# Performance work log

Hardware: AMD Instinct MI355X
Metric: run time of the kernel (lower is better)

The kernel has to match this reference:

```python
import jax, jax.numpy as jnp
import numpy as np

TAU = 0.1
EPS_FREQ = 1e-06
EPS_DENOM = 1e-12


def _l2norm(x, eps=1e-12):
    # matches F.normalize(p=2, dim=-1)
    n = jnp.linalg.norm(x, axis=-1, keepdims=True)
    return x / jnp.maximum(n, eps)


def setup_inputs() -> dict:
    key = jax.random.key(0)
    k1, k2, k3, k4, k5 = jax.random.split(key, 5)
    N, D, C = 4096, 128, 64
    return {
        "protos": jax.random.normal(k1, (C, D), dtype=jnp.float32),
        "proj2": jax.random.normal(k2, (N, D), dtype=jnp.float32),
        "target2": jax.random.randint(k3, (N,), 0, C, dtype=jnp.int64),
        "proj3": jax.random.normal(k4, (N, D), dtype=jnp.float32),
        "target3": jax.random.randint(k5, (N,), 0, C, dtype=jnp.int64),
    }


def reference(protos, proj2, target2, proj3, target3):
    feats = _l2norm(jnp.concatenate([proj2, proj3], axis=0))        # [M, D]
    labels = jnp.concatenate([target2, target3], axis=0)             # [M]
    protos_n = _l2norm(protos)                                       # [C, D]
    M = feats.shape[0]
    C = protos_n.shape[0]

    sim = jnp.matmul(feats, feats.T) / TAU                           # [M, M]
    proto_sim = jnp.matmul(feats, protos_n.T) / TAU                  # [M, C]

    eye = jnp.eye(M, dtype=bool)
    exp_sim = jnp.where(eye, 0.0, jnp.exp(sim))                      # diag masked to -inf -> exp 0
    exp_proto = jnp.exp(proto_sim)

    match = labels[:, None] == labels[None, :]                       # [M, M]
    numer_region = jnp.sum(exp_sim * match, axis=1)                  # [M]
    numer_proto = jnp.take_along_axis(exp_proto, labels[:, None], axis=1)[:, 0]
    numer = numer_region + numer_proto

    # bincount(labels ++ arange(C)) == per-class count + 1
    cls_freq = jnp.zeros((C,), dtype=jnp.float32).at[labels].add(1.0) + 1.0 + EPS_FREQ
    feat_w = cls_freq[labels]                                        # [M], per-row weight

    denom_region = jnp.sum(exp_sim, axis=1) / feat_w                 # row-constant weight; diag already 0
    denom_proto = jnp.sum(exp_proto / cls_freq[None, :], axis=1)
    denom = denom_region + denom_proto

    loss = -jnp.log(numer / (denom + EPS_DENOM))
    return jnp.mean(loss)
```

## Files before the change

kernel.cpp:

```cpp
#include <hip/hip_runtime.h>
#include <math.h>
#include <stdint.h>

#define D    128
#define CCLS 64
#define CH   16

typedef _Float16 f16x8 __attribute__((ext_vector_type(8)));
typedef float    f32x4 __attribute__((ext_vector_type(4)));

__device__ __forceinline__ float wave_reduce_sum(float v) {
    #pragma unroll
    for (int off = 32; off > 0; off >>= 1) v += __shfl_xor(v, off, 64);
    return v;
}

__device__ __forceinline__ void gload_lds16(const void* g, void* l) {
    __builtin_amdgcn_global_load_lds(
        (const __attribute__((address_space(1))) uint32_t*)g,
        (__attribute__((address_space(3))) uint32_t*)l, 16, 0, 0);
}
__device__ __forceinline__ void gload_lds4(const void* g, void* l) {
    __builtin_amdgcn_global_load_lds(
        (const __attribute__((address_space(1))) uint32_t*)g,
        (__attribute__((address_space(3))) uint32_t*)l, 4, 0, 0);
}

__global__ void norm_kernel(const float* __restrict__ protos,
                            const float* __restrict__ proj2,
                            const float* __restrict__ proj3,
                            const int* __restrict__ t2, const int* __restrict__ t3,
                            _Float16* __restrict__ ftile, int* __restrict__ labs,
                            float* __restrict__ cls_freq, float* __restrict__ loss_sum,
                            int* __restrict__ ticket, int N, int M) {
    const float SCL = 3.8017368953f;
    int w = threadIdx.x >> 6;
    int lane = threadIdx.x & 63;
    int row = blockIdx.x * (blockDim.x >> 6) + w;
    const int MT = M + 128;

    if (blockIdx.x == 0) {
        __shared__ int h[CCLS];
        int t = threadIdx.x;
        if (t < CCLS) h[t] = 0;
        if (t == 0) { loss_sum[0] = 0.f; ticket[0] = 0; }
        __syncthreads();
        for (int i = t; i < M; i += blockDim.x) {
            int lab = (i < N) ? t2[i] : t3[i - N];
            atomicAdd(&h[lab], 1);
        }
        __syncthreads();
        if (t < CCLS) cls_freq[t] = (float)h[t] + 1.0f + 1e-6f;
    }

    if (row < MT) {
        const float* src = nullptr;
        if (row < M)             src = (row < N) ? proj2 + (size_t)row * D
                                                 : proj3 + (size_t)(row - N) * D;
        else if (row < M + CCLS) src = protos + (size_t)(row - M) * D;
        float2 v = {0.f, 0.f};
        if (src) v = ((const float2*)src)[lane];
        float ss = wave_reduce_sum(v.x * v.x + v.y * v.y);
        float scale = src ? SCL / fmaxf(sqrtf(ss), 1e-12f) : 0.f;
        _Float16 h0 = (_Float16)(v.x * scale), h1 = (_Float16)(v.y * scale);
        int k0 = 2 * lane;
        size_t off = ((size_t)(row >> 4) * 16 + (k0 >> 3)) * 128 + (row & 15) * 8 + (k0 & 7);
        ftile[off] = h0; ftile[off + 1] = h1;
        if (row < M && lane == 0)
            labs[row] = (row < N) ? t2[row] : t3[row - N];
    }
}

__global__ __launch_bounds__(256, 4)
void sim_kernel(const _Float16* __restrict__ ftile,
                const int* __restrict__ labs,
                const float* __restrict__ cls_freq,
                float* __restrict__ nPart, float* __restrict__ dPart,
                float* __restrict__ rp, int M) {
    __shared__ _Float16 sbuf[2][8320];

    const int panel = blockIdx.x;
    const int chunk = blockIdx.y;
    const int t = threadIdx.x;
    const int w = t >> 6, lane = t & 63;
    const int g = lane >> 4, li = lane & 15;
    const int lo = g * 128 + li * 8;
    const int rtA = panel * 8 + w * 2;
    const int nS = (M / 64) / CH;
    const int sBase = chunk * nS;
    const int row0 = panel * 128 + 32 * w + li;
    const int rl0 = labs[row0];
    const int rl1 = labs[row0 + 16];

    f16x8 a[2][4];
    #pragma unroll
    for (int m = 0; m < 2; ++m)
        #pragma unroll
        for (int kt = 0; kt < 4; ++kt)
            a[m][kt] = *(const f16x8*)(ftile + (size_t)(rtA + m) * 2048 + kt * 512 + lo);

    float rn[2] = {0.f, 0.f}, rd[2] = {0.f, 0.f};
    float rpacc[2] = {0.f, 0.f};

    #define STAGE(buf, s)                                                        \
        {                                                                        \
            const char* bsrc_ = (const char*)ftile + (size_t)(s) * 16384;        \
            char* dst_ = (char*)&sbuf[(buf)][0];                                 \
            _Pragma("unroll")                                                    \
            for (int q = 0; q < 4; ++q) {                                        \
                int j_ = w * 4 + q;                                              \
                gload_lds16(bsrc_ + (size_t)j_ * 1024 + lane * 16,               \
                            dst_ + (size_t)j_ * 1024);                           \
            }                                                                    \
            if (w == 0)                                                          \
                gload_lds4((const char*)labs + (size_t)(s) * 256 + lane * 4,     \
                           dst_ + 16384);                                        \
        }

    STAGE(0, sBase);
    __syncthreads();
    int cur = 0;

    const int diagS = 2 * panel + (w >> 1);
    const int nD0 = 2 * (w & 1);

    for (int si = 0; si < nS; ++si) {
        const int s = sBase + si;
        if (si + 1 < nS) STAGE(cur ^ 1, sBase + si + 1);

        const _Float16* Bl = &sbuf[cur][0];
        const int* clabL = (const int*)&sbuf[cur][8192];
        const bool isDiag = (s == diagS);

        #pragma unroll
        for (int n = 0; n < 4; ++n) {
            f16x8 bn[4];
            #pragma unroll
            for (int kt = 0; kt < 4; ++kt)
                bn[kt] = *(const f16x8*)(Bl + n * 2048 + kt * 512 + lo);

            f32x4 acc[2];
            #pragma unroll
            for (int m = 0; m < 2; ++m)
                #pragma unroll
                for (int r = 0; r < 4; ++r) acc[m][r] = 0.f;

            #pragma unroll
            for (int kt = 0; kt < 4; ++kt)
                #pragma unroll
                for (int m = 0; m < 2; ++m)
                    acc[m] = __builtin_amdgcn_mfma_f32_16x16x32_f16(bn[kt], a[m][kt], acc[m], 0, 0, 0);

            if (isDiag) {
                #pragma unroll
                for (int m = 0; m < 2; ++m)
                    #pragma unroll
                    for (int r = 0; r < 4; ++r)
                        acc[m][r] = (n == nD0 + m && 4 * g + r == li) ? -1e5f : acc[m][r];
            }

            int4 c4 = *(const int4*)(clabL + 16 * n + 4 * g);
            #pragma unroll
            for (int m = 0; m < 2; ++m) {
                float e0 = __builtin_amdgcn_exp2f(acc[m][0]);
                float e1 = __builtin_amdgcn_exp2f(acc[m][1]);
                float e2 = __builtin_amdgcn_exp2f(acc[m][2]);
                float e3 = __builtin_amdgcn_exp2f(acc[m][3]);
                const int rl = m ? rl1 : rl0;
                rd[m] += e0 + e1 + e2 + e3;
                rn[m] += (c4.x == rl) ? e0 : 0.f;
                rn[m] += (c4.y == rl) ? e1 : 0.f;
                rn[m] += (c4.z == rl) ? e2 : 0.f;
                rn[m] += (c4.w == rl) ? e3 : 0.f;
            }
        }

        __syncthreads();
        cur ^= 1;
    }

    if (chunk == 0) {
        const int rbp = M >> 4;
        #pragma unroll
        for (int n = 0; n < 4; ++n) {
            f16x8 bn[4];
            #pragma unroll
            for (int kt = 0; kt < 4; ++kt)
                bn[kt] = *(const f16x8*)(ftile + (size_t)(rbp + n) * 2048 + kt * 512 + lo);
            f32x4 acc[2];
            #pragma unroll
            for (int m = 0; m < 2; ++m)
                #pragma unroll
                for (int r = 0; r < 4; ++r) acc[m][r] = 0.f;
            #pragma unroll
            for (int kt = 0; kt < 4; ++kt)
                #pragma unroll
                for (int m = 0; m < 2; ++m)
                    acc[m] = __builtin_amdgcn_mfma_f32_16x16x32_f16(bn[kt], a[m][kt], acc[m], 0, 0, 0);

            f32x4 fr = *(const f32x4*)(cls_freq + 16 * n + 4 * g);
            const int c0 = 16 * n + 4 * g;
            #pragma unroll
            for (int m = 0; m < 2; ++m) {
                float e0 = __builtin_amdgcn_exp2f(acc[m][0]);
                float e1 = __builtin_amdgcn_exp2f(acc[m][1]);
                float e2 = __builtin_amdgcn_exp2f(acc[m][2]);
                float e3 = __builtin_amdgcn_exp2f(acc[m][3]);
                const int rl = m ? rl1 : rl0;
                rpacc[m] += e0 / fr[0] + e1 / fr[1] + e2 / fr[2] + e3 / fr[3];
                rn[m] += (c0 + 0 == rl) ? e0 : 0.f;
                rn[m] += (c0 + 1 == rl) ? e1 : 0.f;
                rn[m] += (c0 + 2 == rl) ? e2 : 0.f;
                rn[m] += (c0 + 3 == rl) ? e3 : 0.f;
            }
        }
    }

    #pragma unroll
    for (int m = 0; m < 2; ++m) {
        rn[m] += __shfl_xor(rn[m], 16, 64); rn[m] += __shfl_xor(rn[m], 32, 64);
        rd[m] += __shfl_xor(rd[m], 16, 64); rd[m] += __shfl_xor(rd[m], 32, 64);
        if (chunk == 0) {
            rpacc[m] += __shfl_xor(rpacc[m], 16, 64);
            rpacc[m] += __shfl_xor(rpacc[m], 32, 64);
        }
    }
    if (lane < 16) {
        #pragma unroll
        for (int m = 0; m < 2; ++m) {
            const int rowm = row0 + 16 * m;
            nPart[(size_t)chunk * M + rowm] = rn[m];
            dPart[(size_t)chunk * M + rowm] = rd[m];
            if (chunk == 0) rp[rowm] = rpacc[m];
        }
    }
}

__global__ void fin_kernel(const int* __restrict__ labs,
                           const float* __restrict__ cls_freq,
                           const float* __restrict__ nPart,
                           const float* __restrict__ dPart,
                           const float* __restrict__ rp,
                           float* __restrict__ loss_sum, int* __restrict__ ticket,
                           float* __restrict__ out, int M) {
    int i = blockIdx.x * blockDim.x + threadIdx.x;
    float l = 0.f;
    if (i < M) {
        float rnT = 0.f, rdT = 0.f;
        #pragma unroll
        for (int ch = 0; ch < CH; ++ch) {
            rnT += nPart[(size_t)ch * M + i];
            rdT += dPart[(size_t)ch * M + i];
        }
        float denom = rdT / cls_freq[labs[i]] + rp[i];
        l = logf(denom + 1e-12f) - logf(rnT);
    }
    l = wave_reduce_sum(l);
    __shared__ float ws_[4];
    if ((threadIdx.x & 63) == 0) ws_[threadIdx.x >> 6] = l;
    __syncthreads();
    if (threadIdx.x == 0) {
        atomicAdd(loss_sum, ws_[0] + ws_[1] + ws_[2] + ws_[3]);
        __threadfence();
        int old = atomicAdd(ticket, 1);
        if (old == (int)gridDim.x - 1) {
            __threadfence();
            out[0] = *(volatile float*)loss_sum / (float)M;
        }
    }
}

extern "C" void kernel_launch(void* const* d_in, const int* in_sizes, int n_in,
                              void* d_out, int out_size, void* d_ws, size_t ws_size,
                              hipStream_t stream) {
    const float* protos = (const float*)d_in[0];
    const float* proj2  = (const float*)d_in[1];
    const int*   t2     = (const int*)d_in[2];
    const float* proj3  = (const float*)d_in[3];
    const int*   t3     = (const int*)d_in[4];
    float* out = (float*)d_out;

    const int N = in_sizes[1] / D;
    const int M = 2 * N;
    const int MT = M + 128;

    _Float16* ftile = (_Float16*)d_ws;
    int*   labs     = (int*)(ftile + (size_t)MT * D);
    float* cls_freq = (float*)(labs + M);
    float* nPart    = cls_freq + CCLS;
    float* dPart    = nPart + (size_t)CH * M;
    float* rp       = dPart + (size_t)CH * M;
    float* loss_sum = rp + M;
    int*   ticket   = (int*)(loss_sum + 1);

    norm_kernel<<<(MT + 3) / 4, 256, 0, stream>>>(protos, proj2, proj3, t2, t3,
                                                  ftile, labs, cls_freq, loss_sum,
                                                  ticket, N, M);
    dim3 grid(M / 128, CH);
    sim_kernel<<<grid, 256, 0, stream>>>(ftile, labs, cls_freq, nPart, dPart, rp, M);
    fin_kernel<<<(M + 255) / 256, 256, 0, stream>>>(labs, cls_freq, nPart, dPart, rp,
                                                    loss_sum, ticket, out, M);
}
```

Before: 38.55 us.

## Triple-buffer half-tile staging with vmcnt waits and split class histogram

```diff
diff --git a/kernel.cpp b/kernel.cpp
--- a/kernel.cpp
+++ b/kernel.cpp
@@ -5,6 +5,7 @@
 #define D    128
 #define CCLS 64
 #define CH   16
+#define HB   8
 
 typedef _Float16 f16x8 __attribute__((ext_vector_type(8)));
 typedef float    f32x4 __attribute__((ext_vector_type(4)));
@@ -31,7 +32,7 @@
                             const float* __restrict__ proj3,
                             const int* __restrict__ t2, const int* __restrict__ t3,
                             _Float16* __restrict__ ftile, int* __restrict__ labs,
-                            float* __restrict__ cls_freq, float* __restrict__ loss_sum,
+                            float* __restrict__ hpart, float* __restrict__ loss_sum,
                             int* __restrict__ ticket, int N, int M) {
     const float SCL = 3.8017368953f;
     int w = threadIdx.x >> 6;
@@ -39,19 +40,21 @@
     int row = blockIdx.x * (blockDim.x >> 6) + w;
     const int MT = M + 128;
 
-    if (blockIdx.x == 0) {
+    if (blockIdx.x < HB) {
         __shared__ int h[CCLS];
         int t = threadIdx.x;
         if (t < CCLS) h[t] = 0;
-        if (t == 0) { loss_sum[0] = 0.f; ticket[0] = 0; }
         __syncthreads();
-        for (int i = t; i < M; i += blockDim.x) {
-            int lab = (i < N) ? t2[i] : t3[i - N];
+        int base = blockIdx.x * (M / HB);
+        for (int i = t; i < M / HB; i += (int)blockDim.x) {
+            int gi = base + i;
+            int lab = (gi < N) ? t2[gi] : t3[gi - N];
             atomicAdd(&h[lab], 1);
         }
         __syncthreads();
-        if (t < CCLS) cls_freq[t] = (float)h[t] + 1.0f + 1e-6f;
-    }
+        if (t < CCLS) hpart[blockIdx.x * CCLS + t] = (float)h[t];
+    }
+    if (blockIdx.x == HB && threadIdx.x == 0) { loss_sum[0] = 0.f; ticket[0] = 0; }
 
     if (row < MT) {
         const float* src = nullptr;
@@ -74,10 +77,11 @@
 __global__ __launch_bounds__(256, 4)
 void sim_kernel(const _Float16* __restrict__ ftile,
                 const int* __restrict__ labs,
-                const float* __restrict__ cls_freq,
+                const float* __restrict__ hpart,
                 float* __restrict__ nPart, float* __restrict__ dPart,
                 float* __restrict__ rp, int M) {
-    __shared__ _Float16 sbuf[2][8320];
+    __shared__ _Float16 bbuf[3][4096];
+    __shared__ int labL[512];
 
     const int panel = blockIdx.x;
     const int chunk = blockIdx.y;
@@ -86,8 +90,8 @@
     const int g = lane >> 4, li = lane & 15;
     const int lo = g * 128 + li * 8;
     const int rtA = panel * 8 + w * 2;
-    const int nS = (M / 64) / CH;
-    const int sBase = chunk * nS;
+    const int nH = 16;
+    const int sBase = chunk * 8;
     const int row0 = panel * 128 + 32 * w + li;
     const int rl0 = labs[row0];
     const int rl1 = labs[row0 + 16];
@@ -100,44 +104,49 @@
             a[m][kt] = *(const f16x8*)(ftile + (size_t)(rtA + m) * 2048 + kt * 512 + lo);
 
     float rn[2] = {0.f, 0.f}, rd[2] = {0.f, 0.f};
-    float rpacc[2] = {0.f, 0.f};
-
-    #define STAGE(buf, s)                                                        \
-        {                                                                        \
-            const char* bsrc_ = (const char*)ftile + (size_t)(s) * 16384;        \
-            char* dst_ = (char*)&sbuf[(buf)][0];                                 \
-            _Pragma("unroll")                                                    \
-            for (int q = 0; q < 4; ++q) {                                        \
-                int j_ = w * 4 + q;                                              \
-                gload_lds16(bsrc_ + (size_t)j_ * 1024 + lane * 16,               \
-                            dst_ + (size_t)j_ * 1024);                           \
-            }                                                                    \
-            if (w == 0)                                                          \
-                gload_lds4((const char*)labs + (size_t)(s) * 256 + lane * 4,     \
-                           dst_ + 16384);                                        \
-        }
-
-    STAGE(0, sBase);
-    __syncthreads();
-    int cur = 0;
+
+    {
+        const char* lsrc = (const char*)labs + (size_t)sBase * 256;
+        #pragma unroll
+        for (int c = 0; c < 2; ++c) {
+            int cc = w * 2 + c;
+            gload_lds4(lsrc + cc * 256 + lane * 4, (char*)labL + cc * 256);
+        }
+    }
+    #define STAGE_H(buf, h)                                                       \
+        {                                                                         \
+            const char* src_ = (const char*)ftile + (size_t)sBase * 16384         \
+                               + (size_t)(h) * 8192;                              \
+            char* dst_ = (char*)&bbuf[(buf)][0];                                  \
+            _Pragma("unroll")                                                     \
+            for (int c = 0; c < 2; ++c) {                                         \
+                int j_ = w * 2 + c;                                               \
+                gload_lds16(src_ + (size_t)j_ * 1024 + lane * 16,                 \
+                            dst_ + (size_t)j_ * 1024);                            \
+            }                                                                     \
+        }
+    STAGE_H(0, 0);
+    STAGE_H(1, 1);
 
     const int diagS = 2 * panel + (w >> 1);
     const int nD0 = 2 * (w & 1);
 
-    for (int si = 0; si < nS; ++si) {
-        const int s = sBase + si;
-        if (si + 1 < nS) STAGE(cur ^ 1, sBase + si + 1);
-
-        const _Float16* Bl = &sbuf[cur][0];
-        const int* clabL = (const int*)&sbuf[cur][8192];
+    for (int h = 0; h < nH; ++h) {
+        if (h < nH - 1) { asm volatile("s_waitcnt vmcnt(2)" ::: "memory"); }
+        else            { asm volatile("s_waitcnt vmcnt(0)" ::: "memory"); }
+        __builtin_amdgcn_s_barrier();
+
+        const _Float16* Bl = &bbuf[h % 3][0];
+        const int s = sBase + (h >> 1);
         const bool isDiag = (s == diagS);
-
-        #pragma unroll
-        for (int n = 0; n < 4; ++n) {
+        const int nBase = (h & 1) * 2;
+
+        #pragma unroll
+        for (int nl = 0; nl < 2; ++nl) {
             f16x8 bn[4];
             #pragma unroll
             for (int kt = 0; kt < 4; ++kt)
-                bn[kt] = *(const f16x8*)(Bl + n * 2048 + kt * 512 + lo);
+                bn[kt] = *(const f16x8*)(Bl + nl * 2048 + kt * 512 + lo);
 
             f32x4 acc[2];
             #pragma unroll
@@ -156,10 +165,11 @@
                 for (int m = 0; m < 2; ++m)
                     #pragma unroll
                     for (int r = 0; r < 4; ++r)
-                        acc[m][r] = (n == nD0 + m && 4 * g + r == li) ? -1e5f : acc[m][r];
+                        acc[m][r] = (nBase + nl == nD0 + m && 4 * g + r == li)
+                                    ? -1e5f : acc[m][r];
             }
 
-            int4 c4 = *(const int4*)(clabL + 16 * n + 4 * g);
+            int4 c4 = *(const int4*)(labL + h * 32 + nl * 16 + 4 * g);
             #pragma unroll
             for (int m = 0; m < 2; ++m) {
                 float e0 = __builtin_amdgcn_exp2f(acc[m][0]);
@@ -175,10 +185,10 @@
             }
         }
 
-        __syncthreads();
-        cur ^= 1;
-    }
-
+        if (h + 2 < nH) STAGE_H((h + 2) % 3, h + 2);
+    }
+
+    float rpacc[2] = {0.f, 0.f};
     if (chunk == 0) {
         const int rbp = M >> 4;
         #pragma unroll
@@ -198,7 +208,10 @@
                 for (int m = 0; m < 2; ++m)
                     acc[m] = __builtin_amdgcn_mfma_f32_16x16x32_f16(bn[kt], a[m][kt], acc[m], 0, 0, 0);
 
-            f32x4 fr = *(const f32x4*)(cls_freq + 16 * n + 4 * g);
+            f32x4 fr = {1.0f + 1e-6f, 1.0f + 1e-6f, 1.0f + 1e-6f, 1.0f + 1e-6f};
+            #pragma unroll
+            for (int b = 0; b < HB; ++b)
+                fr += *(const f32x4*)(hpart + b * CCLS + 16 * n + 4 * g);
             const int c0 = 16 * n + 4 * g;
             #pragma unroll
             for (int m = 0; m < 2; ++m) {
@@ -237,7 +250,7 @@
 }
 
 __global__ void fin_kernel(const int* __restrict__ labs,
-                           const float* __restrict__ cls_freq,
+                           const float* __restrict__ hpart,
                            const float* __restrict__ nPart,
                            const float* __restrict__ dPart,
                            const float* __restrict__ rp,
@@ -252,7 +265,11 @@
             rnT += nPart[(size_t)ch * M + i];
             rdT += dPart[(size_t)ch * M + i];
         }
-        float denom = rdT / cls_freq[labs[i]] + rp[i];
+        int lab = labs[i];
+        float fsum = 1.0f + 1e-6f;
+        #pragma unroll
+        for (int b = 0; b < HB; ++b) fsum += hpart[b * CCLS + lab];
+        float denom = rdT / fsum + rp[i];
         l = logf(denom + 1e-12f) - logf(rnT);
     }
     l = wave_reduce_sum(l);
@@ -286,18 +303,18 @@
 
     _Float16* ftile = (_Float16*)d_ws;
     int*   labs     = (int*)(ftile + (size_t)MT * D);
-    float* cls_freq = (float*)(labs + M);
-    float* nPart    = cls_freq + CCLS;
+    float* hpart    = (float*)(labs + M);
+    float* nPart    = hpart + HB * CCLS;
     float* dPart    = nPart + (size_t)CH * M;
     float* rp       = dPart + (size_t)CH * M;
     float* loss_sum = rp + M;
     int*   ticket   = (int*)(loss_sum + 1);
 
     norm_kernel<<<(MT + 3) / 4, 256, 0, stream>>>(protos, proj2, proj3, t2, t3,
-                                                  ftile, labs, cls_freq, loss_sum,
+                                                  ftile, labs, hpart, loss_sum,
                                                   ticket, N, M);
     dim3 grid(M / 128, CH);
-    sim_kernel<<<grid, 256, 0, stream>>>(ftile, labs, cls_freq, nPart, dPart, rp, M);
-    fin_kernel<<<(M + 255) / 256, 256, 0, stream>>>(labs, cls_freq, nPart, dPart, rp,
+    sim_kernel<<<grid, 256, 0, stream>>>(ftile, labs, hpart, nPart, dPart, rp, M);
+    fin_kernel<<<(M + 255) / 256, 256, 0, stream>>>(labs, hpart, nPart, dPart, rp,
                                                     loss_sum, ticket, out, M);
 }
```

New measurement: 37.65 us, median of 2. 2.4% less time.
